# Kernel tuning notes

Measured on AMD Instinct MI355X. Metric: run time of the kernel, lower is better.

Reference implementation:

```python
import jax, jax.numpy as jnp
import numpy as np

N_BATCH = 1024   # batch size (P=256 identities x K=4 instances)
M_PARTS = 8      # local stripes per image
D_FEAT = 128     # local feature dim
K_PER_ID = 4
MARGIN = 0.3
EPS = 1e-12


def setup_inputs() -> dict:
    key = jax.random.key(0)
    inputs = jax.random.normal(key, (N_BATCH, M_PARTS, D_FEAT), dtype=jnp.float32)
    labels = jnp.arange(N_BATCH, dtype=jnp.int64) // K_PER_ID  # equal samples per class
    return {"inputs": inputs, "labels": labels}


def _shortest_dist(dmat):
    """DTW-style monotone shortest path over the (m, n) grid.
    dmat: [m, n, N, N] -> returns [N, N].
    """
    m = dmat.shape[0]
    # first row: only moves to the right -> cumulative sum over j
    row = jnp.cumsum(dmat[0], axis=0)  # [n, N, N]
    inf = jnp.full(dmat.shape[2:], jnp.inf, dtype=dmat.dtype)

    def step(carry, inp):
        d_ij, up = inp                       # each [N, N]
        val = jnp.minimum(carry, up) + d_ij  # carry=inf at j=0 -> picks `up`
        return val, val

    for i in range(1, m):  # m is a small structural constant (stripes)
        _, row = jax.lax.scan(step, inf, (dmat[i], row))
    return row[-1]  # dist[m-1][n-1], shape [N, N]


def _local_dist(x):
    """x: [N, m, d] (already L2-normalized) -> pairwise aligned dist [N, N]."""
    N, m, d = x.shape
    xf = x.reshape(N * m, d)
    sq = jnp.sum(xf * xf, axis=1)
    dist = sq[:, None] + sq[None, :] - 2.0 * (xf @ xf.T)   # [Nm, Nm]
    dist = jnp.sqrt(jnp.clip(dist, EPS, None))
    dist = jnp.tanh(dist * 0.5)  # (e^d - 1) / (e^d + 1)
    dist = dist.reshape(N, m, N, m).transpose(1, 3, 0, 2)   # [m, n, N, N]
    return _shortest_dist(dist)


def reference(inputs, labels):
    # normalize local features to unit length
    x = inputs / (jnp.linalg.norm(inputs, axis=-1, keepdims=True) + EPS)
    dist_mat = _local_dist(x)  # [N, N]

    # hard example mining
    is_pos = labels[:, None] == labels[None, :]
    dist_ap = jnp.max(jnp.where(is_pos, dist_mat, -jnp.inf), axis=1)
    dist_an = jnp.min(jnp.where(is_pos, jnp.inf, dist_mat), axis=1)

    # MarginRankingLoss(margin)(dist_an, dist_ap, y=1)
    loss = jnp.mean(jnp.maximum(dist_ap - dist_an + MARGIN, 0.0))
    return loss
```

## Files before the change

### kernel.cpp

```cpp
#include <hip/hip_runtime.h>
#include <hip/hip_bf16.h>
#include <math.h>

#define NB 1024
#define MP 8
#define DF 128
#define NV (NB*MP)
#define EPSR 1e-12f
#define MARGIN_ 0.3f

#define GC0  0.4999965f
#define GC1 -0.0416276f
#define GC2  0.0040808f
#define GC3 -0.00035138f
#define GC4  0.00001765f

typedef __bf16    bf16x8 __attribute__((ext_vector_type(8)));
typedef float     f32x4  __attribute__((ext_vector_type(4)));
typedef __fp16    fp16x2 __attribute__((ext_vector_type(2)));
typedef _Float16  f16x8  __attribute__((ext_vector_type(8)));

__device__ __forceinline__ void async_copy16(const void* g, void* l) {
    __builtin_amdgcn_global_load_lds(
        (const __attribute__((address_space(1))) void*)g,
        (__attribute__((address_space(3))) void*)l,
        16, 0, 0);
}

__global__ __launch_bounds__(256) void norm_kernel(const float* __restrict__ x,
                                                   unsigned short* __restrict__ xnb,
                                                   unsigned* __restrict__ ap_max,
                                                   unsigned* __restrict__ an_min) {
    if (blockIdx.x == 0) {
        for (int i = threadIdx.x; i < NB; i += 256) {
            ap_max[i] = 0u;
            an_min[i] = 0x7F800000u;
        }
    }
    const int wave = threadIdx.x >> 6;
    const int lane = threadIdx.x & 63;
    const int v = blockIdx.x * 4 + wave;
    const float e0 = x[v * DF + lane];
    const float e1 = x[v * DF + 64 + lane];
    float s = e0 * e0 + e1 * e1;
    #pragma unroll
    for (int off = 32; off > 0; off >>= 1) s += __shfl_xor(s, off);
    const float inv = 1.0f / (sqrtf(s) + EPSR);
    const __hip_bfloat16 b0 = __float2bfloat16(e0 * inv);
    const __hip_bfloat16 b1 = __float2bfloat16(e1 * inv);
    xnb[v * DF + lane]      = *(const unsigned short*)&b0;
    xnb[v * DF + 64 + lane] = *(const unsigned short*)&b1;
}

__global__ __launch_bounds__(256) void dist_kernel(const unsigned short* __restrict__ xnb,
                                                   const int* __restrict__ labels,
                                                   unsigned* __restrict__ ap_max,
                                                   unsigned* __restrict__ an_min) {
    __shared__ alignas(16) unsigned char smem[32768];
    unsigned short* As = (unsigned short*)smem;
    unsigned short* Bs = (unsigned short*)(smem + 16384);
    unsigned short* E  = (unsigned short*)smem;

    const int idx = (int)blockIdx.x;
    float fsq = sqrtf(8.0f * (float)idx + 1.0f);
    int by = (int)((fsq - 1.0f) * 0.5f);
    while ((by + 1) * (by + 2) / 2 <= idx) ++by;
    while (by * (by + 1) / 2 > idx) --by;
    const int bx = idx - by * (by + 1) / 2;

    const int t    = threadIdx.x;
    const int wave = t >> 6;
    const int lane = t & 63;
    const int wr   = wave >> 1;
    const int wc   = wave & 1;
    const int aBase = bx * 16;
    const int bBase = by * 16;

    const int fr = lane & 15;
    const int fq = lane >> 4;

    f32x4 acc[4][4];
    #pragma unroll
    for (int tr = 0; tr < 4; ++tr)
        #pragma unroll
        for (int tc = 0; tc < 4; ++tc) acc[tr][tc] = (f32x4){0.f, 0.f, 0.f, 0.f};

    #pragma unroll
    for (int kci = 0; kci < 2; ++kci) {
        const int kc = kci * 64;
        if (kci) __syncthreads();
        #pragma unroll
        for (int i = 0; i < 8; ++i) {
            const int ldi  = t + i * 256;
            const int side = ldi >> 10;
            const int slot = ldi & 1023;
            const int r    = slot >> 3;
            const int pos  = slot & 7;
            const int ch   = pos ^ (r & 7);
            const int gv   = (side ? bBase : aBase) * MP + r;
            const void* g = &xnb[gv * DF + kc + ch * 8];
            void* l = side ? (void*)&Bs[slot * 8] : (void*)&As[slot * 8];
            async_copy16(g, l);
        }
        __syncthreads();

        #pragma unroll
        for (int ksl = 0; ksl < 2; ++ksl) {
            bf16x8 af[4], bfr[4];
            const int ch = ksl * 4 + fq;
            #pragma unroll
            for (int tr = 0; tr < 4; ++tr) {
                const int va = wr * 64 + tr * 16 + fr;
                af[tr] = *(const bf16x8*)&As[va * 64 + ((ch ^ (fr & 7)) * 8)];
            }
            #pragma unroll
            for (int tc = 0; tc < 4; ++tc) {
                const int vb = wc * 64 + tc * 16 + fr;
                bfr[tc] = *(const bf16x8*)&Bs[vb * 64 + ((ch ^ (fr & 7)) * 8)];
            }
            #pragma unroll
            for (int tr = 0; tr < 4; ++tr)
                #pragma unroll
                for (int tc = 0; tc < 4; ++tc)
                    acc[tr][tc] = __builtin_amdgcn_mfma_f32_16x16x32_bf16(
                        af[tr], bfr[tc], acc[tr][tc], 0, 0, 0);
        }
    }
    __syncthreads();

    #pragma unroll
    for (int tr = 0; tr < 4; ++tr) {
        const int r0   = wr * 64 + tr * 16 + fq * 4;
        const int aL   = r0 >> 3;
        const int half = fq & 1;
        #pragma unroll
        for (int tc = 0; tc < 4; ++tc) {
            const int c  = wc * 64 + tc * 16 + fr;
            const int bL = c >> 3, j = c & 7;
            float td[4];
            #pragma unroll
            for (int g = 0; g < 4; ++g) {
                const float d2 = fmaxf(fmaf(-2.0f, acc[tr][tc][g], 2.0f), 0.0f);
                const float d  = __builtin_amdgcn_sqrtf(d2);
                const float pg = fmaf(fmaf(fmaf(fmaf(GC4, d2, GC3), d2, GC2),
                                           d2, GC1), d2, GC0);
                td[g] = d * pg;
            }
            const fp16x2 h01 = __builtin_amdgcn_cvt_pkrtz(td[0], td[1]);
            const fp16x2 h23 = __builtin_amdgcn_cvt_pkrtz(td[2], td[3]);
            uint2 w;
            w.x = __builtin_bit_cast(unsigned, h01);
            w.y = __builtin_bit_cast(unsigned, h23);
            const int p   = (aL << 4) + bL;
            const int pos = j ^ (bL & 7);
            *(uint2*)&E[(p << 6) + (pos << 3) + (half << 2)] = w;
        }
    }
    __syncthreads();

    f16x8 colv[8];
    {
        const int s = t & 7;
        #pragma unroll
        for (int j = 0; j < 8; ++j)
            colv[j] = *(const f16x8*)&E[(t << 6) + ((j ^ s) << 3)];
    }

    float rowv[8];
    {
        float c = 0.0f;
        #pragma unroll
        for (int j = 0; j < 8; ++j) { c += (float)colv[j][0]; rowv[j] = c; }
    }
    #pragma unroll
    for (int i = 1; i < 8; ++i) {
        float carry = INFINITY;
        #pragma unroll
        for (int j = 0; j < 8; ++j) {
            const float v = fminf(carry, rowv[j]) + (float)colv[j][i];
            rowv[j] = v;
            carry = v;
        }
    }
    const float d = rowv[7];

    const int aG = aBase + (t >> 4);
    const int bG = bBase + (t & 15);
    const bool pos = (labels[aG] == labels[bG]);

    float an_v = pos ? INFINITY : d;
    float ap_v = pos ? d : 0.0f;
    #pragma unroll
    for (int off = 1; off <= 8; off <<= 1) {
        an_v = fminf(an_v, __shfl_xor(an_v, off));
        ap_v = fmaxf(ap_v, __shfl_xor(ap_v, off));
    }
    if ((t & 15) == 0) {
        atomicMin(&an_min[aG], __float_as_uint(an_v));
        if (ap_v > 0.0f) atomicMax(&ap_max[aG], __float_as_uint(ap_v));
    }

    if (bx != by) {
        float an_m = pos ? INFINITY : d;
        float ap_m = pos ? d : 0.0f;
        an_m = fminf(an_m, __shfl_xor(an_m, 16));
        an_m = fminf(an_m, __shfl_xor(an_m, 32));
        ap_m = fmaxf(ap_m, __shfl_xor(ap_m, 16));
        ap_m = fmaxf(ap_m, __shfl_xor(ap_m, 32));
        if (lane < 16) {
            const int bG2 = bBase + lane;
            atomicMin(&an_min[bG2], __float_as_uint(an_m));
            if (ap_m > 0.0f) atomicMax(&ap_max[bG2], __float_as_uint(ap_m));
        }
    }
}

__global__ __launch_bounds__(256) void loss_kernel(const unsigned* __restrict__ ap_max,
                                                   const unsigned* __restrict__ an_min,
                                                   float* __restrict__ out) {
    __shared__ float buf[4];
    const int wave = threadIdx.x >> 6;
    const int lane = threadIdx.x & 63;
    float s = 0.0f;
    for (int i = threadIdx.x; i < NB; i += 256) {
        const float ap = __uint_as_float(ap_max[i]);
        const float an = __uint_as_float(an_min[i]);
        s += fmaxf(ap - an + MARGIN_, 0.0f);
    }
    #pragma unroll
    for (int off = 32; off > 0; off >>= 1) s += __shfl_xor(s, off);
    if (lane == 0) buf[wave] = s;
    __syncthreads();
    if (threadIdx.x == 0) {
        out[0] = (buf[0] + buf[1] + buf[2] + buf[3]) * (1.0f / (float)NB);
    }
}

extern "C" void kernel_launch(void* const* d_in, const int* in_sizes, int n_in,
                              void* d_out, int out_size, void* d_ws, size_t ws_size,
                              hipStream_t stream) {
    const float* x      = (const float*)d_in[0];
    const int*   labels = (const int*)d_in[1];
    float* out = (float*)d_out;

    unsigned short* xnb = (unsigned short*)d_ws;
    unsigned* ap_max = (unsigned*)(xnb + (size_t)NV * DF);
    unsigned* an_min = ap_max + NB;

    const int ntiles = (NB / 16) * (NB / 16 + 1) / 2;

    norm_kernel<<<NV / 4, 256, 0, stream>>>(x, xnb, ap_max, an_min);
    dist_kernel<<<ntiles, 256, 0, stream>>>(xnb, labels, ap_max, an_min);
    loss_kernel<<<1, 256, 0, stream>>>(ap_max, an_min, out);
}
```

Baseline: 87.04 us.

## Split each distance tile into two half-width blocks with padded LDS layout

Each 16x16 image-pair tile is split along the B dimension into two blocks of 16x8 images, doubling the grid. Each block then holds fewer accumulators per wave, a smaller LDS footprint and fewer B rows, which aims to raise occupancy and spread work across more CUs. The staging buffer for the alignment DP switches to a padded stride to ease bank conflicts. In exchange, the A tile is loaded twice from global memory, and only half the threads take part in the DP and reduction phase.

Result: no change. 88.10 us (+1.2%).

```diff
diff --git a/kernel.cpp b/kernel.cpp
--- a/kernel.cpp
+++ b/kernel.cpp
@@ -15,10 +15,12 @@
 #define GC3 -0.00035138f
 #define GC4  0.00001765f
 
+#define ESTRIDE 68
+
 typedef __bf16    bf16x8 __attribute__((ext_vector_type(8)));
 typedef float     f32x4  __attribute__((ext_vector_type(4)));
 typedef __fp16    fp16x2 __attribute__((ext_vector_type(2)));
-typedef _Float16  f16x8  __attribute__((ext_vector_type(8)));
+typedef _Float16  f16x4  __attribute__((ext_vector_type(4)));
 
 __device__ __forceinline__ void async_copy16(const void* g, void* l) {
     __builtin_amdgcn_global_load_lds(
@@ -56,12 +58,13 @@
                                                    const int* __restrict__ labels,
                                                    unsigned* __restrict__ ap_max,
                                                    unsigned* __restrict__ an_min) {
-    __shared__ alignas(16) unsigned char smem[32768];
+    __shared__ alignas(16) unsigned char smem[24576];
     unsigned short* As = (unsigned short*)smem;
     unsigned short* Bs = (unsigned short*)(smem + 16384);
     unsigned short* E  = (unsigned short*)smem;
 
-    const int idx = (int)blockIdx.x;
+    const int idx = (int)blockIdx.x >> 1;
+    const int h   = (int)blockIdx.x & 1;
     float fsq = sqrtf(8.0f * (float)idx + 1.0f);
     int by = (int)((fsq - 1.0f) * 0.5f);
     while ((by + 1) * (by + 2) / 2 <= idx) ++by;
@@ -71,17 +74,15 @@
     const int t    = threadIdx.x;
     const int wave = t >> 6;
     const int lane = t & 63;
-    const int wr   = wave >> 1;
-    const int wc   = wave & 1;
     const int aBase = bx * 16;
-    const int bBase = by * 16;
+    const int bBase = by * 16 + h * 8;
 
     const int fr = lane & 15;
     const int fq = lane >> 4;
 
-    f32x4 acc[4][4];
-    #pragma unroll
-    for (int tr = 0; tr < 4; ++tr)
+    f32x4 acc[2][4];
+    #pragma unroll
+    for (int tr = 0; tr < 2; ++tr)
         #pragma unroll
         for (int tc = 0; tc < 4; ++tc) acc[tr][tc] = (f32x4){0.f, 0.f, 0.f, 0.f};
 
@@ -90,36 +91,36 @@
         const int kc = kci * 64;
         if (kci) __syncthreads();
         #pragma unroll
-        for (int i = 0; i < 8; ++i) {
-            const int ldi  = t + i * 256;
-            const int side = ldi >> 10;
-            const int slot = ldi & 1023;
-            const int r    = slot >> 3;
-            const int pos  = slot & 7;
-            const int ch   = pos ^ (r & 7);
-            const int gv   = (side ? bBase : aBase) * MP + r;
-            const void* g = &xnb[gv * DF + kc + ch * 8];
-            void* l = side ? (void*)&Bs[slot * 8] : (void*)&As[slot * 8];
-            async_copy16(g, l);
+        for (int i = 0; i < 6; ++i) {
+            const int ldi = t + i * 256;
+            int slot, r, gvbase;
+            unsigned short* base;
+            if (i < 4) {
+                slot = ldi; r = slot >> 3; gvbase = aBase * MP; base = As;
+            } else {
+                slot = ldi - 1024; r = slot >> 3; gvbase = bBase * MP; base = Bs;
+            }
+            const int ch = (slot & 7) ^ (r & 7);
+            async_copy16(&xnb[(gvbase + r) * DF + kc + ch * 8], &base[slot * 8]);
         }
         __syncthreads();
 
         #pragma unroll
         for (int ksl = 0; ksl < 2; ++ksl) {
-            bf16x8 af[4], bfr[4];
+            bf16x8 af[2], bfr[4];
             const int ch = ksl * 4 + fq;
             #pragma unroll
-            for (int tr = 0; tr < 4; ++tr) {
-                const int va = wr * 64 + tr * 16 + fr;
+            for (int tr = 0; tr < 2; ++tr) {
+                const int va = wave * 32 + tr * 16 + fr;
                 af[tr] = *(const bf16x8*)&As[va * 64 + ((ch ^ (fr & 7)) * 8)];
             }
             #pragma unroll
             for (int tc = 0; tc < 4; ++tc) {
-                const int vb = wc * 64 + tc * 16 + fr;
+                const int vb = tc * 16 + fr;
                 bfr[tc] = *(const bf16x8*)&Bs[vb * 64 + ((ch ^ (fr & 7)) * 8)];
             }
             #pragma unroll
-            for (int tr = 0; tr < 4; ++tr)
+            for (int tr = 0; tr < 2; ++tr)
                 #pragma unroll
                 for (int tc = 0; tc < 4; ++tc)
                     acc[tr][tc] = __builtin_amdgcn_mfma_f32_16x16x32_bf16(
@@ -129,13 +130,12 @@
     __syncthreads();
 
     #pragma unroll
-    for (int tr = 0; tr < 4; ++tr) {
-        const int r0   = wr * 64 + tr * 16 + fq * 4;
-        const int aL   = r0 >> 3;
+    for (int tr = 0; tr < 2; ++tr) {
+        const int aL   = 4 * wave + 2 * tr + (fq >> 1);
         const int half = fq & 1;
         #pragma unroll
         for (int tc = 0; tc < 4; ++tc) {
-            const int c  = wc * 64 + tc * 16 + fr;
+            const int c  = tc * 16 + fr;
             const int bL = c >> 3, j = c & 7;
             float td[4];
             #pragma unroll
@@ -151,66 +151,71 @@
             uint2 w;
             w.x = __builtin_bit_cast(unsigned, h01);
             w.y = __builtin_bit_cast(unsigned, h23);
-            const int p   = (aL << 4) + bL;
-            const int pos = j ^ (bL & 7);
-            *(uint2*)&E[(p << 6) + (pos << 3) + (half << 2)] = w;
+            const int p   = aL * 8 + bL;
+            const int pos = j ^ bL;
+            *(uint2*)&E[p * ESTRIDE + pos * 8 + half * 4] = w;
         }
     }
     __syncthreads();
 
-    f16x8 colv[8];
-    {
-        const int s = t & 7;
-        #pragma unroll
-        for (int j = 0; j < 8; ++j)
-            colv[j] = *(const f16x8*)&E[(t << 6) + ((j ^ s) << 3)];
-    }
-
-    float rowv[8];
-    {
-        float c = 0.0f;
-        #pragma unroll
-        for (int j = 0; j < 8; ++j) { c += (float)colv[j][0]; rowv[j] = c; }
-    }
-    #pragma unroll
-    for (int i = 1; i < 8; ++i) {
-        float carry = INFINITY;
+    if (t < 128) {
+        const int bL = t & 7;
+        f16x4 lo[8], hi[8];
         #pragma unroll
         for (int j = 0; j < 8; ++j) {
-            const float v = fminf(carry, rowv[j]) + (float)colv[j][i];
-            rowv[j] = v;
-            carry = v;
-        }
-    }
-    const float d = rowv[7];
-
-    const int aG = aBase + (t >> 4);
-    const int bG = bBase + (t & 15);
-    const bool pos = (labels[aG] == labels[bG]);
-
-    float an_v = pos ? INFINITY : d;
-    float ap_v = pos ? d : 0.0f;
-    #pragma unroll
-    for (int off = 1; off <= 8; off <<= 1) {
-        an_v = fminf(an_v, __shfl_xor(an_v, off));
-        ap_v = fmaxf(ap_v, __shfl_xor(ap_v, off));
-    }
-    if ((t & 15) == 0) {
-        atomicMin(&an_min[aG], __float_as_uint(an_v));
-        if (ap_v > 0.0f) atomicMax(&ap_max[aG], __float_as_uint(ap_v));
-    }
-
-    if (bx != by) {
-        float an_m = pos ? INFINITY : d;
-        float ap_m = pos ? d : 0.0f;
-        an_m = fminf(an_m, __shfl_xor(an_m, 16));
-        an_m = fminf(an_m, __shfl_xor(an_m, 32));
-        ap_m = fmaxf(ap_m, __shfl_xor(ap_m, 16));
-        ap_m = fmaxf(ap_m, __shfl_xor(ap_m, 32));
-        if (lane < 16) {
-            const int bG2 = bBase + lane;
-            atomicMin(&an_min[bG2], __float_as_uint(an_m));
-            if (ap_m > 0.0f) atomicMax(&ap_max[bG2], __float_as_uint(ap_m));
+            const int base = t * ESTRIDE + ((j ^ bL) * 8);
+            lo[j] = *(const f16x4*)&E[base];
+            hi[j] = *(const f16x4*)&E[base + 4];
+        }
+
+        float rowv[8];
+        {
+            float c = 0.0f;
+            #pragma unroll
+            for (int j = 0; j < 8; ++j) { c += (float)lo[j][0]; rowv[j] = c; }
+        }
+        #pragma unroll
+        for (int i = 1; i < 8; ++i) {
+            float carry = INFINITY;
+            #pragma unroll
+            for (int j = 0; j < 8; ++j) {
+                const float e = (i < 4) ? (float)lo[j][i] : (float)hi[j][i - 4];
+                const float v = fminf(carry, rowv[j]) + e;
+                rowv[j] = v;
+                carry = v;
+            }
+        }
+        const float d = rowv[7];
+
+        const int aG = aBase + (t >> 3);
+        const int bG = bBase + bL;
+        const bool pos = (labels[aG] == labels[bG]);
+
+        float an_v = pos ? INFINITY : d;
+        float ap_v = pos ? d : 0.0f;
+        #pragma unroll
+        for (int off = 1; off <= 4; off <<= 1) {
+            an_v = fminf(an_v, __shfl_xor(an_v, off));
+            ap_v = fmaxf(ap_v, __shfl_xor(ap_v, off));
+        }
+        if (bL == 0) {
+            atomicMin(&an_min[aG], __float_as_uint(an_v));
+            if (ap_v > 0.0f) atomicMax(&ap_max[aG], __float_as_uint(ap_v));
+        }
+
+        if (bx != by) {
+            float an_m = pos ? INFINITY : d;
+            float ap_m = pos ? d : 0.0f;
+            #pragma unroll
+            for (int off = 8; off <= 32; off <<= 1) {
+                an_m = fminf(an_m, __shfl_xor(an_m, off));
+                ap_m = fmaxf(ap_m, __shfl_xor(ap_m, off));
+            }
+            if ((lane >> 3) == 0) {
+                const int bG2 = bBase + (lane & 7);
+                atomicMin(&an_min[bG2], __float_as_uint(an_m));
+                if (ap_m > 0.0f) atomicMax(&ap_max[bG2], __float_as_uint(ap_m));
+            }
         }
     }
 }
@@ -250,6 +255,6 @@
     const int ntiles = (NB / 16) * (NB / 16 + 1) / 2;
 
     norm_kernel<<<NV / 4, 256, 0, stream>>>(x, xnb, ap_max, an_min);
-    dist_kernel<<<ntiles, 256, 0, stream>>>(xnb, labels, ap_max, an_min);
+    dist_kernel<<<ntiles * 2, 256, 0, stream>>>(xnb, labels, ap_max, an_min);
     loss_kernel<<<1, 256, 0, stream>>>(ap_max, an_min, out);
 }
```
